# Kernel optimization log

Hardware: AMD Instinct MI355X
Metric: run time of the kernel (lower is better)

## Reference

```python
import jax, jax.numpy as jnp
import numpy as np
from jax import lax

N_NODES = 100000
N_EDGES = 1600000
NUM_GRAPHS = 2000
F_IN = 64
HIDDEN = 64
NUM_LAYERS = 3
K = 7
NUM_CLASSES = 10


def setup_inputs() -> dict:
    key = jax.random.key(0)
    ks = jax.random.split(key, 16)
    x = jax.random.normal(ks[0], (N_NODES, F_IN), jnp.float32)
    edge_index = jax.random.randint(ks[1], (2, N_EDGES), 0, N_NODES)
    batch = jnp.sort(jax.random.randint(ks[2], (N_NODES,), 0, NUM_GRAPHS))
    s = 1.0 / np.sqrt(HIDDEN)
    p = lambda k_, sh: jax.random.uniform(k_, sh, jnp.float32, -s, s)
    return dict(
        x=x, edge_index=edge_index, batch=batch,
        W1l=p(ks[3], (F_IN, HIDDEN)), b1=p(ks[4], (HIDDEN,)), W1r=p(ks[5], (F_IN, HIDDEN)),
        W2l=p(ks[6], (HIDDEN, HIDDEN)), b2=p(ks[7], (HIDDEN,)), W2r=p(ks[8], (HIDDEN, HIDDEN)),
        W3l=p(ks[9], (HIDDEN, HIDDEN)), b3=p(ks[10], (HIDDEN,)), W3r=p(ks[11], (HIDDEN, HIDDEN)),
        conv1d_w=p(ks[12], (32, HIDDEN, NUM_LAYERS)), conv1d_b=jnp.zeros((32,), jnp.float32),
        lin1_w=p(ks[13], (32 * (K - NUM_LAYERS + 1), HIDDEN)), lin1_b=jnp.zeros((HIDDEN,), jnp.float32),
        lin2_w=p(ks[14], (HIDDEN, NUM_CLASSES)), lin2_b=jnp.zeros((NUM_CLASSES,), jnp.float32),
    )


def _sage(x, src, dst, Wl, b, Wr):
    # PyG SAGEConv (aggr='mean'): lin_l(mean_j x_j) + lin_r(x_i); lin_l carries the bias.
    n = x.shape[0]
    msum = jax.ops.segment_sum(x[src], dst, num_segments=n)          # [N, D] gather+scatter
    cnt = jax.ops.segment_sum(jnp.ones((src.shape[0],), x.dtype), dst, num_segments=n)
    mean = msum / jnp.maximum(cnt, 1.0)[:, None]
    return mean @ Wl + b + x @ Wr


def _sort_pool(x, batch, num_graphs, k):
    # SortAggregation: per graph, sort nodes descending by last feature channel,
    # keep top-k, zero-pad short graphs, flatten to [B, k*D].
    N, D = x.shape
    perm = jnp.lexsort((-x[:, -1], batch))  # primary: graph id, secondary: desc last channel
    sb = batch[perm]
    counts = jax.ops.segment_sum(jnp.ones((N,), jnp.int32), batch, num_segments=num_graphs)
    starts = jnp.concatenate([jnp.zeros((1,), jnp.int32), jnp.cumsum(counts)[:-1]])
    rank = jnp.arange(N, dtype=jnp.int32) - starts[sb]
    valid = rank < k
    b_idx = jnp.where(valid, sb, num_graphs)  # route overflow nodes to dummy row
    r_idx = jnp.where(valid, rank, 0)
    out = jnp.zeros((num_graphs + 1, k, D), x.dtype).at[b_idx, r_idx].set(x[perm])
    return out[:num_graphs].reshape(num_graphs, k * D)


def reference(x, edge_index, batch, W1l, b1, W1r, W2l, b2, W2r, W3l, b3, W3r,
              conv1d_w, conv1d_b, lin1_w, lin1_b, lin2_w, lin2_b):
    src, dst = edge_index[0], edge_index[1]
    h = jax.nn.relu(_sage(x, src, dst, W1l, b1, W1r))
    h = jax.nn.relu(_sage(h, src, dst, W2l, b2, W2r))
    h = jax.nn.relu(_sage(h, src, dst, W3l, b3, W3r))
    g = _sort_pool(h, batch, NUM_GRAPHS, K)                       # [B, K*H]
    g = g.reshape(NUM_GRAPHS, K, HIDDEN).transpose(0, 2, 1)       # [B, H, K]
    c = lax.conv_general_dilated(g, conv1d_w, (1,), 'VALID',
                                 dimension_numbers=('NCH', 'OIH', 'NCH'))
    c = jax.nn.relu(c + conv1d_b[None, :, None])                  # [B, 32, K-ks+1]
    flat = c.reshape(NUM_GRAPHS, -1)
    h1 = jax.nn.relu(flat @ lin1_w + lin1_b)                      # dropout = identity (eval)
    logits = h1 @ lin2_w + lin2_b
    return jax.nn.log_softmax(logits, axis=-1)
```

## Files before the change

kernel.cpp:

```cpp
#include <hip/hip_runtime.h>
#include <hip/hip_bf16.h>

#define NN 100000
#define NE 1600000
#define NG 2000
#define KTOP 7

#define BNODES 128
#define NBKT 782
#define EPB 8192
#define NL1B 196
#define L2CAP 4096

__global__ void k_gstart(const int* __restrict__ bat, int* __restrict__ gstart) {
    int g = blockIdx.x * blockDim.x + threadIdx.x;
    if (g > NG) return;
    int lo = 0, hi = NN;
    while (lo < hi) { int mid = (lo + hi) >> 1; if (bat[mid] < g) lo = mid + 1; else hi = mid; }
    gstart[g] = lo;
}

__global__ __launch_bounds__(256) void k_bcount(const int* __restrict__ edst,
                                                int* __restrict__ bh) {
    __shared__ int h[NBKT];
    int t = threadIdx.x, bk = blockIdx.x;
    for (int q = t; q < NBKT; q += 256) h[q] = 0;
    __syncthreads();
    int e0 = bk * EPB, e1 = min(e0 + EPB, NE);
    for (int e = e0 + t; e < e1; e += 256) atomicAdd(&h[edst[e] >> 7], 1);
    __syncthreads();
    for (int q = t; q < NBKT; q += 256) bh[bk * NBKT + q] = h[q];
}

__global__ void k_colscan(int* __restrict__ bh, int* __restrict__ btot) {
    __shared__ int carry;
    int b = blockIdx.x, t = threadIdx.x;
    if (t == 0) carry = 0;
    __syncthreads();
    for (int base = 0; base < NL1B; base += 64) {
        int idx = base + t;
        int v = (idx < NL1B) ? bh[idx * NBKT + b] : 0;
        int x = v;
        #pragma unroll
        for (int off = 1; off < 64; off <<= 1) {
            int y = __shfl_up(x, off);
            if (t >= off) x += y;
        }
        int c = carry;
        if (idx < NL1B) bh[idx * NBKT + b] = c + x - v;
        __syncthreads();
        if (t == 63) carry = c + x;
        __syncthreads();
    }
    if (t == 0) btot[b] = carry;
}

__global__ void k_btscan(const int* __restrict__ btot, int* __restrict__ bstart) {
    __shared__ int s[1024];
    int t = threadIdx.x;
    int v = (t < NBKT) ? btot[t] : 0;
    s[t] = v; __syncthreads();
    for (int off = 1; off < 1024; off <<= 1) {
        int y = (t >= off) ? s[t - off] : 0;
        __syncthreads();
        s[t] += y;
        __syncthreads();
    }
    if (t < NBKT) bstart[t] = s[t] - v;
    if (t == NBKT - 1) bstart[NBKT] = s[t];
}

__global__ __launch_bounds__(256) void k_bscatter(const int* __restrict__ esrc,
        const int* __restrict__ edst, const int* __restrict__ bh,
        const int* __restrict__ bstart, int* __restrict__ ebuf) {
    __shared__ int cur[NBKT];
    int t = threadIdx.x, bk = blockIdx.x;
    for (int q = t; q < NBKT; q += 256) cur[q] = bstart[q] + bh[bk * NBKT + q];
    __syncthreads();
    int e0 = bk * EPB, e1 = min(e0 + EPB, NE);
    for (int e = e0 + t; e < e1; e += 256) {
        int d = edst[e], s = esrc[e];
        int pos = atomicAdd(&cur[d >> 7], 1);
        ebuf[pos] = s | ((d & 127) << 20);
    }
}

__global__ __launch_bounds__(128) void k_bbuild(const int* __restrict__ ebuf,
        const int* __restrict__ bstart, int* __restrict__ ce, int* __restrict__ ptr) {
    __shared__ int lord[L2CAP];
    __shared__ int cnt[BNODES], sc[BNODES], cursor[BNODES];
    int b = blockIdx.x, t = threadIdx.x;
    int base = bstart[b], nb = bstart[b + 1] - base;
    cnt[t] = 0;
    __syncthreads();
    for (int j = t; j < nb; j += 128) atomicAdd(&cnt[ebuf[base + j] >> 20], 1);
    __syncthreads();
    int v = cnt[t]; sc[t] = v; __syncthreads();
    for (int off = 1; off < 128; off <<= 1) {
        int y = (t >= off) ? sc[t - off] : 0;
        __syncthreads();
        sc[t] += y;
        __syncthreads();
    }
    int segend = sc[t], segstart = sc[t] - v;
    cursor[t] = segstart;
    __syncthreads();
    bool fits = (nb <= L2CAP);
    for (int j = t; j < nb; j += 128) {
        int pv = ebuf[base + j];
        int node = pv >> 20;
        int pos = atomicAdd(&cursor[node], 1);
        if (fits) lord[pos] = pv & 0xFFFFF;
        else ce[base + pos] = pv & 0xFFFFF;
    }
    __syncthreads();
    if (fits) {
        for (int a = segstart + 1; a < segend; ++a) {
            int val = lord[a]; int j = a - 1;
            while (j >= segstart && lord[j] > val) { lord[j + 1] = lord[j]; --j; }
            lord[j + 1] = val;
        }
        __syncthreads();
        for (int j = t; j < nb; j += 128) ce[base + j] = lord[j];
    } else {
        for (int a = segstart + 1; a < segend; ++a) {
            int val = ce[base + a]; int j = a - 1;
            while (j >= segstart && ce[base + j] > val) { ce[base + j + 1] = ce[base + j]; --j; }
            ce[base + j + 1] = val;
        }
    }
    int node = b * BNODES + t;
    if (node <= NN) ptr[node] = base + segstart;
}

#define FMA4C(av, B, acc) do { \
    acc[0] = fmaf(av, B.x, acc[0]); acc[1] = fmaf(av, B.y, acc[1]); \
    acc[2] = fmaf(av, B.z, acc[2]); acc[3] = fmaf(av, B.w, acc[3]); } while (0)

__global__ __launch_bounds__(256) void k_gemm(const float* __restrict__ X,
        const float* __restrict__ Wl, const float* __restrict__ Wr,
        const float* __restrict__ bias,
        float* __restrict__ XL, float* __restrict__ T, int n) {
    __shared__ float As[64][68];
    __shared__ float Bl[64][64];
    __shared__ float Br[64][64];
    int t = threadIdx.x;
    int n0 = blockIdx.x * 64;

    #pragma unroll
    for (int q = 0; q < 4; ++q) {
        int idx = t + q * 256;
        ((float4*)&Bl[0][0])[idx] = ((const float4*)Wl)[idx];
        ((float4*)&Br[0][0])[idx] = ((const float4*)Wr)[idx];
    }
    #pragma unroll
    for (int q = 0; q < 4; ++q) {
        int f = t + q * 256;
        int node = f >> 4, seg = f & 15;
        int g = n0 + node;
        float4 v = make_float4(0.f, 0.f, 0.f, 0.f);
        if (g < n) v = *(const float4*)&X[(size_t)g * 64 + seg * 4];
        *(float4*)&As[node][seg * 4] = v;
    }
    __syncthreads();

    int ty4 = (t >> 4) * 4, tx4 = (t & 15) * 4;
    float accl[4][4] = {{0.f}}, accr[4][4] = {{0.f}};
    for (int kc = 0; kc < 64; kc += 4) {
        float4 Av[4], L[4], R[4];
        #pragma unroll
        for (int i = 0; i < 4; ++i) Av[i] = *(const float4*)&As[ty4 + i][kc];
        #pragma unroll
        for (int j = 0; j < 4; ++j) {
            L[j] = *(const float4*)&Bl[kc + j][tx4];
            R[j] = *(const float4*)&Br[kc + j][tx4];
        }
        #pragma unroll
        for (int i = 0; i < 4; ++i) {
            FMA4C(Av[i].x, L[0], accl[i]); FMA4C(Av[i].y, L[1], accl[i]);
            FMA4C(Av[i].z, L[2], accl[i]); FMA4C(Av[i].w, L[3], accl[i]);
            FMA4C(Av[i].x, R[0], accr[i]); FMA4C(Av[i].y, R[1], accr[i]);
            FMA4C(Av[i].z, R[2], accr[i]); FMA4C(Av[i].w, R[3], accr[i]);
        }
    }
    float b0 = bias[tx4 + 0], b1v = bias[tx4 + 1], b2v = bias[tx4 + 2], b3v = bias[tx4 + 3];
    #pragma unroll
    for (int i = 0; i < 4; ++i) {
        int g = n0 + ty4 + i;
        if (g < n) {
            *(float4*)&XL[(size_t)g * 64 + tx4] =
                make_float4(accl[i][0], accl[i][1], accl[i][2], accl[i][3]);
            *(float4*)&T[(size_t)g * 64 + tx4] =
                make_float4(accr[i][0] + b0, accr[i][1] + b1v, accr[i][2] + b2v, accr[i][3] + b3v);
        }
    }
}

__global__ __launch_bounds__(256) void k_aggregate(const float* __restrict__ XL,
        float* __restrict__ Hout, const int* __restrict__ ptr, const int* __restrict__ ce,
        int n, float* __restrict__ key) {
    int wave = threadIdx.x >> 6, lane = threadIdx.x & 63;
    int i = blockIdx.x * 4 + wave;
    if (i >= n) return;
    int s = ptr[i], e = ptr[i + 1];
    int g = lane >> 4;
    int c4 = (lane & 15) * 4;
    float4 acc = make_float4(0.f, 0.f, 0.f, 0.f);
    int a = s;
    for (; a + 16 <= e; a += 16) {
        int r0 = ce[a + g], r1 = ce[a + 4 + g], r2 = ce[a + 8 + g], r3 = ce[a + 12 + g];
        float4 v0 = *(const float4*)&XL[(size_t)r0 * 64 + c4];
        float4 v1 = *(const float4*)&XL[(size_t)r1 * 64 + c4];
        float4 v2 = *(const float4*)&XL[(size_t)r2 * 64 + c4];
        float4 v3 = *(const float4*)&XL[(size_t)r3 * 64 + c4];
        acc.x += (v0.x + v1.x) + (v2.x + v3.x);
        acc.y += (v0.y + v1.y) + (v2.y + v3.y);
        acc.z += (v0.z + v1.z) + (v2.z + v3.z);
        acc.w += (v0.w + v1.w) + (v2.w + v3.w);
    }
    for (; a + 4 <= e; a += 4) {
        int r0 = ce[a + g];
        float4 v0 = *(const float4*)&XL[(size_t)r0 * 64 + c4];
        acc.x += v0.x; acc.y += v0.y; acc.z += v0.z; acc.w += v0.w;
    }
    if (g < e - a) {
        int r0 = ce[a + g];
        float4 v0 = *(const float4*)&XL[(size_t)r0 * 64 + c4];
        acc.x += v0.x; acc.y += v0.y; acc.z += v0.z; acc.w += v0.w;
    }
    #pragma unroll
    for (int off = 16; off < 64; off <<= 1) {
        acc.x += __shfl_xor(acc.x, off);
        acc.y += __shfl_xor(acc.y, off);
        acc.z += __shfl_xor(acc.z, off);
        acc.w += __shfl_xor(acc.w, off);
    }
    if (g == 0) {
        float cm = fmaxf((float)(e - s), 1.f);
        float4 tv = *(const float4*)&Hout[(size_t)i * 64 + c4];
        float4 h;
        h.x = fmaxf(acc.x / cm + tv.x, 0.f);
        h.y = fmaxf(acc.y / cm + tv.y, 0.f);
        h.z = fmaxf(acc.z / cm + tv.z, 0.f);
        h.w = fmaxf(acc.w / cm + tv.w, 0.f);
        *(float4*)&Hout[(size_t)i * 64 + c4] = h;
        if (key && (lane & 15) == 15) key[i] = h.w;
    }
}

__global__ __launch_bounds__(256) void k_topk(const float* __restrict__ key,
        const int* __restrict__ gstart, int* __restrict__ idx7, int G) {
    int wv = threadIdx.x >> 6, lane = threadIdx.x & 63;
    int b = blockIdx.x * 4 + wv;
    if (b >= G) return;
    int s = gstart[b], e = gstart[b + 1];
    float pk = 3.4e38f; int pi = -1;
    for (int r = 0; r < KTOP; ++r) {
        float bk = -1.f; int bi = -1;
        for (int i = s + lane; i < e; i += 64) {
            float k = key[i];
            bool elig = (k < pk) || (k == pk && i > pi);
            if (elig && (k > bk || (k == bk && (unsigned)i < (unsigned)bi))) { bk = k; bi = i; }
        }
        #pragma unroll
        for (int off = 1; off < 64; off <<= 1) {
            float ok = __shfl_xor(bk, off);
            int   oi = __shfl_xor(bi, off);
            if (ok > bk || (ok == bk && (unsigned)oi < (unsigned)bi)) { bk = ok; bi = oi; }
        }
        if (lane == 0) idx7[b * KTOP + r] = bi;
        pk = bk; pi = bi;
    }
}

__global__ __launch_bounds__(256) void k_head(const float* __restrict__ h3,
        const int* __restrict__ idx7,
        const float* __restrict__ cw, const float* __restrict__ cb,
        const float* __restrict__ l1w, const float* __restrict__ l1b,
        const float* __restrict__ l2w, const float* __restrict__ l2b,
        float* __restrict__ out, int G) {
    __shared__ float sw[32 * 64 * 3];
    __shared__ float s2w[64 * 10];
    __shared__ float sg[4][KTOP][64];
    __shared__ float sflat[4][160];
    __shared__ float sh1[4][64];
    __shared__ float slog[4][10];
    int t = threadIdx.x;
    for (int q = t; q < 32 * 64 * 3; q += 256) sw[q] = cw[q];
    for (int q = t; q < 640; q += 256) s2w[q] = l2w[q];
    int wv = t >> 6, lane = t & 63;
    int b = blockIdx.x * 4 + wv;
    for (int r = 0; r < KTOP; ++r) {
        int idx = idx7[b * KTOP + r];
        sg[wv][r][lane] = (idx >= 0) ? h3[(size_t)idx * 64 + lane] : 0.f;
    }
    __syncthreads();
    for (int idx = lane; idx < 160; idx += 64) {
        int o = idx / 5, p = idx % 5;
        float acc = cb[o];
        #pragma unroll
        for (int dt = 0; dt < 3; ++dt) {
            const float* wrow = &sw[(o * 64) * 3 + dt];
            const float* grow = &sg[wv][p + dt][0];
            for (int i = 0; i < 64; ++i) acc = fmaf(wrow[i * 3], grow[i], acc);
        }
        sflat[wv][idx] = fmaxf(acc, 0.f);
    }
    __syncthreads();
    {
        float acc = l1b[lane];
        for (int k = 0; k < 160; ++k) acc = fmaf(sflat[wv][k], l1w[k * 64 + lane], acc);
        sh1[wv][lane] = fmaxf(acc, 0.f);
    }
    __syncthreads();
    if (lane < 10) {
        float acc = l2b[lane];
        for (int k = 0; k < 64; ++k) acc = fmaf(sh1[wv][k], s2w[k * 10 + lane], acc);
        slog[wv][lane] = acc;
    }
    __syncthreads();
    if (lane < 10) {
        float m = -3.4e38f;
        for (int j = 0; j < 10; ++j) m = fmaxf(m, slog[wv][j]);
        float ssum = 0.f;
        for (int j = 0; j < 10; ++j) ssum += expf(slog[wv][j] - m);
        out[b * 10 + lane] = slog[wv][lane] - m - logf(ssum);
    }
}

extern "C" void kernel_launch(void* const* d_in, const int* in_sizes, int n_in,
                              void* d_out, int out_size, void* d_ws, size_t ws_size,
                              hipStream_t stream) {
    const float* x   = (const float*)d_in[0];
    const int*   ei  = (const int*)d_in[1];
    const int*   bat = (const int*)d_in[2];
    const float* W1l = (const float*)d_in[3], *b1 = (const float*)d_in[4], *W1r = (const float*)d_in[5];
    const float* W2l = (const float*)d_in[6], *b2 = (const float*)d_in[7], *W2r = (const float*)d_in[8];
    const float* W3l = (const float*)d_in[9], *b3 = (const float*)d_in[10], *W3r = (const float*)d_in[11];
    const float* cw  = (const float*)d_in[12], *cb  = (const float*)d_in[13];
    const float* l1w = (const float*)d_in[14], *l1b = (const float*)d_in[15];
    const float* l2w = (const float*)d_in[16], *l2b = (const float*)d_in[17];
    float* out = (float*)d_out;
    const int* esrc = ei;
    const int* edst = ei + NE;

    char* w = (char*)d_ws;
    size_t off = 0;
    auto take = [&](size_t bytes) { void* p = w + off; off = (off + bytes + 255) & ~(size_t)255; return p; };
    int*   bh      = (int*)take((size_t)NL1B * NBKT * 4);
    int*   btot    = (int*)take((size_t)NBKT * 4);
    int*   bstart  = (int*)take((size_t)(NBKT + 1) * 4);
    int*   gstart  = (int*)take((size_t)(NG + 1) * 4);
    int*   idx7    = (int*)take((size_t)NG * KTOP * 4);
    int*   ebuf    = (int*)take((size_t)NE * 4);
    int*   csr_ptr = (int*)take((size_t)(NN + 1) * 4);
    int*   csr_e   = (int*)take((size_t)NE * 4);
    float* XL      = (float*)take((size_t)NN * 64 * 4);
    float* Ha      = (float*)take((size_t)NN * 64 * 4);
    float* Hb      = (float*)take((size_t)NN * 64 * 4);
    float* key     = (float*)take((size_t)NN * 4);

    k_bcount <<<NL1B, 256, 0, stream>>>(edst, bh);
    k_gstart <<<(NG + 1 + 255) / 256, 256, 0, stream>>>(bat, gstart);
    k_colscan<<<NBKT, 64, 0, stream>>>(bh, btot);
    k_btscan <<<1, 1024, 0, stream>>>(btot, bstart);
    k_bscatter<<<NL1B, 256, 0, stream>>>(esrc, edst, bh, bstart, ebuf);
    k_bbuild <<<NBKT, 128, 0, stream>>>(ebuf, bstart, csr_e, csr_ptr);

    k_gemm<<<(NN + 63) / 64, 256, 0, stream>>>(x, W1l, W1r, b1, XL, Ha, NN);
    k_aggregate<<<(NN + 3) / 4, 256, 0, stream>>>(XL, Ha, csr_ptr, csr_e, NN, nullptr);
    k_gemm<<<(NN + 63) / 64, 256, 0, stream>>>(Ha, W2l, W2r, b2, XL, Hb, NN);
    k_aggregate<<<(NN + 3) / 4, 256, 0, stream>>>(XL, Hb, csr_ptr, csr_e, NN, nullptr);
    k_gemm<<<(NN + 63) / 64, 256, 0, stream>>>(Hb, W3l, W3r, b3, XL, Ha, NN);
    k_aggregate<<<(NN + 3) / 4, 256, 0, stream>>>(XL, Ha, csr_ptr, csr_e, NN, key);

    k_topk<<<(NG + 3) / 4, 256, 0, stream>>>(key, gstart, idx7, NG);
    k_head<<<NG / 4, 256, 0, stream>>>(Ha, idx7, cw, cb, l1w, l1b, l2w, l2b, out, NG);
}
```

Baseline: 393.1 us.

## Fuse first GEMM with edge bucket count and graph-start search in one launch

Merges the layer-1 GEMM, the edge-bucket histogram and the graph-start binary search into one heterogeneous launch, so independent work runs concurrently and two launches disappear. The GEMM becomes persistent, with 768 blocks looping over tiles and loading the weights once per block. The aggregate kernel now issues its residual load early so it overlaps with the gathers. The cost is fewer GEMM blocks, which may lower occupancy, and a larger shared allocation for the histogram blocks.

Measured after the change: 375.8 us. -4.4%, faster.

```diff
diff --git a/kernel.cpp b/kernel.cpp
--- a/kernel.cpp
+++ b/kernel.cpp
@@ -12,24 +12,109 @@
 #define NL1B 196
 #define L2CAP 4096
 
-__global__ void k_gstart(const int* __restrict__ bat, int* __restrict__ gstart) {
-    int g = blockIdx.x * blockDim.x + threadIdx.x;
-    if (g > NG) return;
-    int lo = 0, hi = NN;
-    while (lo < hi) { int mid = (lo + hi) >> 1; if (bat[mid] < g) lo = mid + 1; else hi = mid; }
-    gstart[g] = lo;
-}
-
-__global__ __launch_bounds__(256) void k_bcount(const int* __restrict__ edst,
-                                                int* __restrict__ bh) {
-    __shared__ int h[NBKT];
-    int t = threadIdx.x, bk = blockIdx.x;
-    for (int q = t; q < NBKT; q += 256) h[q] = 0;
-    __syncthreads();
-    int e0 = bk * EPB, e1 = min(e0 + EPB, NE);
-    for (int e = e0 + t; e < e1; e += 256) atomicAdd(&h[edst[e] >> 7], 1);
-    __syncthreads();
-    for (int q = t; q < NBKT; q += 256) bh[bk * NBKT + q] = h[q];
+#define GEMM_BLOCKS 768
+#define SMEM_FLOATS (64 * 68 + 2 * 64 * 64)
+
+#define FMA4C(av, B, acc) do { \
+    acc[0] = fmaf(av, B.x, acc[0]); acc[1] = fmaf(av, B.y, acc[1]); \
+    acc[2] = fmaf(av, B.z, acc[2]); acc[3] = fmaf(av, B.w, acc[3]); } while (0)
+
+__device__ __forceinline__ void gemm_body(int bid, int nblocks, float* smem,
+        const float* __restrict__ X, const float* __restrict__ Wl,
+        const float* __restrict__ Wr, const float* __restrict__ bias,
+        float* __restrict__ XL, float* __restrict__ T, int n) {
+    float* As = smem;
+    float* Bl = smem + 64 * 68;
+    float* Br = Bl + 64 * 64;
+    int t = threadIdx.x;
+
+    #pragma unroll
+    for (int q = 0; q < 4; ++q) {
+        int idx = t + q * 256;
+        ((float4*)Bl)[idx] = ((const float4*)Wl)[idx];
+        ((float4*)Br)[idx] = ((const float4*)Wr)[idx];
+    }
+    int ty4 = (t >> 4) * 4, tx4 = (t & 15) * 4;
+    float b0 = bias[tx4 + 0], b1v = bias[tx4 + 1], b2v = bias[tx4 + 2], b3v = bias[tx4 + 3];
+    int ntiles = (n + 63) / 64;
+    for (int tile = bid; tile < ntiles; tile += nblocks) {
+        int n0 = tile * 64;
+        #pragma unroll
+        for (int q = 0; q < 4; ++q) {
+            int f = t + q * 256;
+            int node = f >> 4, seg = f & 15;
+            int g = n0 + node;
+            float4 v = make_float4(0.f, 0.f, 0.f, 0.f);
+            if (g < n) v = *(const float4*)&X[(size_t)g * 64 + seg * 4];
+            *(float4*)&As[node * 68 + seg * 4] = v;
+        }
+        __syncthreads();
+        float accl[4][4] = {{0.f}}, accr[4][4] = {{0.f}};
+        for (int kc = 0; kc < 64; kc += 4) {
+            float4 Av[4], L[4], R[4];
+            #pragma unroll
+            for (int i = 0; i < 4; ++i) Av[i] = *(const float4*)&As[(ty4 + i) * 68 + kc];
+            #pragma unroll
+            for (int j = 0; j < 4; ++j) {
+                L[j] = *(const float4*)&Bl[(kc + j) * 64 + tx4];
+                R[j] = *(const float4*)&Br[(kc + j) * 64 + tx4];
+            }
+            #pragma unroll
+            for (int i = 0; i < 4; ++i) {
+                FMA4C(Av[i].x, L[0], accl[i]); FMA4C(Av[i].y, L[1], accl[i]);
+                FMA4C(Av[i].z, L[2], accl[i]); FMA4C(Av[i].w, L[3], accl[i]);
+                FMA4C(Av[i].x, R[0], accr[i]); FMA4C(Av[i].y, R[1], accr[i]);
+                FMA4C(Av[i].z, R[2], accr[i]); FMA4C(Av[i].w, R[3], accr[i]);
+            }
+        }
+        #pragma unroll
+        for (int i = 0; i < 4; ++i) {
+            int g = n0 + ty4 + i;
+            if (g < n) {
+                *(float4*)&XL[(size_t)g * 64 + tx4] =
+                    make_float4(accl[i][0], accl[i][1], accl[i][2], accl[i][3]);
+                *(float4*)&T[(size_t)g * 64 + tx4] =
+                    make_float4(accr[i][0] + b0, accr[i][1] + b1v, accr[i][2] + b2v, accr[i][3] + b3v);
+            }
+        }
+        __syncthreads();
+    }
+}
+
+__global__ __launch_bounds__(256) void k_gemm(const float* __restrict__ X,
+        const float* __restrict__ Wl, const float* __restrict__ Wr,
+        const float* __restrict__ bias,
+        float* __restrict__ XL, float* __restrict__ T, int n) {
+    __shared__ float smem[SMEM_FLOATS];
+    gemm_body(blockIdx.x, GEMM_BLOCKS, smem, X, Wl, Wr, bias, XL, T, n);
+}
+
+__global__ __launch_bounds__(256) void k_front(const float* __restrict__ X,
+        const float* __restrict__ Wl, const float* __restrict__ Wr,
+        const float* __restrict__ bias, float* __restrict__ XL, float* __restrict__ T,
+        const int* __restrict__ edst, int* __restrict__ bh,
+        const int* __restrict__ bat, int* __restrict__ gstart) {
+    __shared__ float smem[SMEM_FLOATS];
+    int bid = blockIdx.x, t = threadIdx.x;
+    if (bid < GEMM_BLOCKS) {
+        gemm_body(bid, GEMM_BLOCKS, smem, X, Wl, Wr, bias, XL, T, NN);
+    } else if (bid < GEMM_BLOCKS + NL1B) {
+        int bk = bid - GEMM_BLOCKS;
+        int* h = (int*)smem;
+        for (int q = t; q < NBKT; q += 256) h[q] = 0;
+        __syncthreads();
+        int e0 = bk * EPB, e1 = min(e0 + EPB, NE);
+        for (int e = e0 + t; e < e1; e += 256) atomicAdd(&h[edst[e] >> 7], 1);
+        __syncthreads();
+        for (int q = t; q < NBKT; q += 256) bh[bk * NBKT + q] = h[q];
+    } else {
+        int g = (bid - GEMM_BLOCKS - NL1B) * 256 + t;
+        if (g <= NG) {
+            int lo = 0, hi = NN;
+            while (lo < hi) { int mid = (lo + hi) >> 1; if (bat[mid] < g) lo = mid + 1; else hi = mid; }
+            gstart[g] = lo;
+        }
+    }
 }
 
 __global__ void k_colscan(int* __restrict__ bh, int* __restrict__ btot) {
@@ -131,69 +216,6 @@
     }
     int node = b * BNODES + t;
     if (node <= NN) ptr[node] = base + segstart;
-}
-
-#define FMA4C(av, B, acc) do { \
-    acc[0] = fmaf(av, B.x, acc[0]); acc[1] = fmaf(av, B.y, acc[1]); \
-    acc[2] = fmaf(av, B.z, acc[2]); acc[3] = fmaf(av, B.w, acc[3]); } while (0)
-
-__global__ __launch_bounds__(256) void k_gemm(const float* __restrict__ X,
-        const float* __restrict__ Wl, const float* __restrict__ Wr,
-        const float* __restrict__ bias,
-        float* __restrict__ XL, float* __restrict__ T, int n) {
-    __shared__ float As[64][68];
-    __shared__ float Bl[64][64];
-    __shared__ float Br[64][64];
-    int t = threadIdx.x;
-    int n0 = blockIdx.x * 64;
-
-    #pragma unroll
-    for (int q = 0; q < 4; ++q) {
-        int idx = t + q * 256;
-        ((float4*)&Bl[0][0])[idx] = ((const float4*)Wl)[idx];
-        ((float4*)&Br[0][0])[idx] = ((const float4*)Wr)[idx];
-    }
-    #pragma unroll
-    for (int q = 0; q < 4; ++q) {
-        int f = t + q * 256;
-        int node = f >> 4, seg = f & 15;
-        int g = n0 + node;
-        float4 v = make_float4(0.f, 0.f, 0.f, 0.f);
-        if (g < n) v = *(const float4*)&X[(size_t)g * 64 + seg * 4];
-        *(float4*)&As[node][seg * 4] = v;
-    }
-    __syncthreads();
-
-    int ty4 = (t >> 4) * 4, tx4 = (t & 15) * 4;
-    float accl[4][4] = {{0.f}}, accr[4][4] = {{0.f}};
-    for (int kc = 0; kc < 64; kc += 4) {
-        float4 Av[4], L[4], R[4];
-        #pragma unroll
-        for (int i = 0; i < 4; ++i) Av[i] = *(const float4*)&As[ty4 + i][kc];
-        #pragma unroll
-        for (int j = 0; j < 4; ++j) {
-            L[j] = *(const float4*)&Bl[kc + j][tx4];
-            R[j] = *(const float4*)&Br[kc + j][tx4];
-        }
-        #pragma unroll
-        for (int i = 0; i < 4; ++i) {
-            FMA4C(Av[i].x, L[0], accl[i]); FMA4C(Av[i].y, L[1], accl[i]);
-            FMA4C(Av[i].z, L[2], accl[i]); FMA4C(Av[i].w, L[3], accl[i]);
-            FMA4C(Av[i].x, R[0], accr[i]); FMA4C(Av[i].y, R[1], accr[i]);
-            FMA4C(Av[i].z, R[2], accr[i]); FMA4C(Av[i].w, R[3], accr[i]);
-        }
-    }
-    float b0 = bias[tx4 + 0], b1v = bias[tx4 + 1], b2v = bias[tx4 + 2], b3v = bias[tx4 + 3];
-    #pragma unroll
-    for (int i = 0; i < 4; ++i) {
-        int g = n0 + ty4 + i;
-        if (g < n) {
-            *(float4*)&XL[(size_t)g * 64 + tx4] =
-                make_float4(accl[i][0], accl[i][1], accl[i][2], accl[i][3]);
-            *(float4*)&T[(size_t)g * 64 + tx4] =
-                make_float4(accr[i][0] + b0, accr[i][1] + b1v, accr[i][2] + b2v, accr[i][3] + b3v);
-        }
-    }
 }
 
 __global__ __launch_bounds__(256) void k_aggregate(const float* __restrict__ XL,
@@ -205,6 +227,7 @@
     int s = ptr[i], e = ptr[i + 1];
     int g = lane >> 4;
     int c4 = (lane & 15) * 4;
+    float4 tv = *(const float4*)&Hout[(size_t)i * 64 + c4];
     float4 acc = make_float4(0.f, 0.f, 0.f, 0.f);
     int a = s;
     for (; a + 16 <= e; a += 16) {
@@ -237,7 +260,6 @@
     }
     if (g == 0) {
         float cm = fmaxf((float)(e - s), 1.f);
-        float4 tv = *(const float4*)&Hout[(size_t)i * 64 + c4];
         float4 h;
         h.x = fmaxf(acc.x / cm + tv.x, 0.f);
         h.y = fmaxf(acc.y / cm + tv.y, 0.f);
@@ -360,18 +382,17 @@
     float* Hb      = (float*)take((size_t)NN * 64 * 4);
     float* key     = (float*)take((size_t)NN * 4);
 
-    k_bcount <<<NL1B, 256, 0, stream>>>(edst, bh);
-    k_gstart <<<(NG + 1 + 255) / 256, 256, 0, stream>>>(bat, gstart);
+    k_front<<<GEMM_BLOCKS + NL1B + 8, 256, 0, stream>>>(x, W1l, W1r, b1, XL, Ha,
+                                                        edst, bh, bat, gstart);
     k_colscan<<<NBKT, 64, 0, stream>>>(bh, btot);
     k_btscan <<<1, 1024, 0, stream>>>(btot, bstart);
     k_bscatter<<<NL1B, 256, 0, stream>>>(esrc, edst, bh, bstart, ebuf);
     k_bbuild <<<NBKT, 128, 0, stream>>>(ebuf, bstart, csr_e, csr_ptr);
 
-    k_gemm<<<(NN + 63) / 64, 256, 0, stream>>>(x, W1l, W1r, b1, XL, Ha, NN);
     k_aggregate<<<(NN + 3) / 4, 256, 0, stream>>>(XL, Ha, csr_ptr, csr_e, NN, nullptr);
-    k_gemm<<<(NN + 63) / 64, 256, 0, stream>>>(Ha, W2l, W2r, b2, XL, Hb, NN);
+    k_gemm<<<GEMM_BLOCKS, 256, 0, stream>>>(Ha, W2l, W2r, b2, XL, Hb, NN);
     k_aggregate<<<(NN + 3) / 4, 256, 0, stream>>>(XL, Hb, csr_ptr, csr_e, NN, nullptr);
-    k_gemm<<<(NN + 63) / 64, 256, 0, stream>>>(Hb, W3l, W3r, b3, XL, Ha, NN);
+    k_gemm<<<GEMM_BLOCKS, 256, 0, stream>>>(Hb, W3l, W3r, b3, XL, Ha, NN);
     k_aggregate<<<(NN + 3) / 4, 256, 0, stream>>>(XL, Ha, csr_ptr, csr_e, NN, key);
 
     k_topk<<<(NG + 3) / 4, 256, 0, stream>>>(key, gstart, idx7, NG);
```
